# Performance work log

Measured on AMD Instinct MI355X. Metric: run time of the kernel, lower is better.

## Reference

```python
import jax, jax.numpy as jnp
import numpy as np

B, N, T, H, W = 4, 256, 4096, 6, 8
SIM_DIM, LOOKUP, OUT_DIM = 128, 101, 128


def setup_inputs() -> dict:
    key = jax.random.key(0)
    k1, k2, k3, k4 = jax.random.split(key, 4)
    x = jax.random.normal(k1, (B, N, T, H, W), dtype=jnp.float32)
    # nn.Linear weights: [out_features, in_features]
    w_proj = jax.random.normal(k2, (SIM_DIM, N), dtype=jnp.float32) * (1.0 / np.sqrt(N))
    w_fc = jax.random.normal(k3, (OUT_DIM, LOOKUP), dtype=jnp.float32) * (1.0 / np.sqrt(LOOKUP))
    b_fc = jax.random.normal(k4, (OUT_DIM,), dtype=jnp.float32) * 0.01
    return {"x": x, "w_proj": w_proj, "w_fc": w_fc, "b_fc": b_fc}


def reference(x, w_proj, w_fc, b_fc):
    # x: [B, N, T, H, W] == torch.stack(inputs, dim=1) for N branch features
    pad = (LOOKUP - 1) // 2
    feat = x.mean(axis=(3, 4))                    # [B, N, T]  spatial mean-pool
    feat = jnp.swapaxes(feat, 1, 2)               # [B, T, N]
    proj = feat @ w_proj.T                        # [B, T, D]  projection (no bias)
    norm = jnp.linalg.norm(proj, axis=2, keepdims=True)
    proj = proj / jnp.maximum(norm, 1e-12)        # F.normalize(p=2, dim=2)
    sims = jnp.einsum('btd,bsd->bts', proj, proj)  # [B, T, T] full pairwise cosine sims
    sims_pad = jnp.pad(sims, ((0, 0), (0, 0), (pad, pad)))  # [B, T, T+w-1]
    # banded gather: band[b,t,j] = sims_pad[b, t, t + j]
    band_idx = jnp.arange(T)[:, None] + jnp.arange(LOOKUP)[None, :]  # [T, w]
    band = jnp.take_along_axis(sims_pad, band_idx[None], axis=2)     # [B, T, w]
    return jax.nn.relu(band @ w_fc.T + b_fc)      # [B, T, OUT_DIM]
```

## Files before the change

kernel.cpp:

```cpp
#include <hip/hip_runtime.h>

#define BB   4
#define NN   256
#define TT   4096
#define DD   128
#define LK   101
#define PADK 50
#define OD   128
#define ROWS 164
#define RSTR 33
#define FSTR 260
#define CPB  8

typedef float vfloat4 __attribute__((ext_vector_type(4)));

__global__ __launch_bounds__(256) void transpose_w_kernel(
    const float* __restrict__ w_proj, const float* __restrict__ w_fc,
    float* __restrict__ w_t, float* __restrict__ wfc_t) {
  int idx = blockIdx.x * 256 + threadIdx.x;
  int stride = gridDim.x * 256;
  for (int i = idx; i < DD * NN; i += stride) {
    int d = i / NN, n = i - d * NN;
    w_t[n * DD + d] = w_proj[i];
  }
  for (int i = idx; i < OD * LK; i += stride) {
    int o = i / LK, j = i - o * LK;
    wfc_t[j * OD + o] = w_fc[i];
  }
}

__global__ __launch_bounds__(256) void pool_kernel(
    const float* __restrict__ x, float* __restrict__ feat) {
  __shared__ float part[2][768];
  int tid = threadIdx.x;
  for (int c = 0; c < CPB; ++c) {
    size_t ck = (size_t)blockIdx.x * CPB + c;
    const vfloat4* x4 = (const vfloat4*)(x + ck * 3072);
    float* pb = part[c & 1];
#pragma unroll
    for (int p = 0; p < 3; ++p) {
      vfloat4 v = __builtin_nontemporal_load(&x4[p * 256 + tid]);
      pb[p * 256 + tid] = v.x + v.y + v.z + v.w;
    }
    __syncthreads();
    if (tid < 64) {
      float s = 0.f;
#pragma unroll
      for (int i = 0; i < 12; ++i) s += pb[tid * 12 + i];
      feat[ck * 64 + tid] = s * (1.0f / 48.0f);
    }
  }
}

__global__ __launch_bounds__(512, 1) void proj_kernel(
    const float* __restrict__ feat, const float* __restrict__ w_t,
    float* __restrict__ projn) {
  extern __shared__ float smemB[];
  float* fs = smemB;
  float* ss = smemB + 64 * FSTR;
  int b = blockIdx.x >> 6;
  int t0 = (blockIdx.x & 63) << 6;
  int tid = threadIdx.x;

  const float* fb = feat + ((size_t)b * NN) * TT + t0;
  for (int i = tid; i < NN * 64; i += 512) {
    int n = i >> 6, u = i & 63;
    fs[u * FSTR + n] = fb[(size_t)n * TT + u];
  }
  __syncthreads();

  int w = tid >> 6, lane = tid & 63;
  int d0u = __builtin_amdgcn_readfirstlane((tid >> 6) * 16);
  float acc[16];
#pragma unroll
  for (int k = 0; k < 16; ++k) acc[k] = 0.f;

  const float* fsr = fs + lane * FSTR;
  for (int n = 0; n < NN; n += 4) {
    float4 f = *(const float4*)(fsr + n);
    const float* wrow = w_t + n * DD + d0u;
#pragma unroll
    for (int q = 0; q < 4; ++q) {
      float fq = (q == 0) ? f.x : (q == 1) ? f.y : (q == 2) ? f.z : f.w;
      const float4* wv4 = (const float4*)(wrow + q * DD);
#pragma unroll
      for (int k = 0; k < 4; ++k) {
        float4 wv = wv4[k];
        acc[4 * k + 0] += wv.x * fq;
        acc[4 * k + 1] += wv.y * fq;
        acc[4 * k + 2] += wv.z * fq;
        acc[4 * k + 3] += wv.w * fq;
      }
    }
  }

  float s2 = 0.f;
#pragma unroll
  for (int k = 0; k < 16; ++k) s2 += acc[k] * acc[k];
  ss[w * 64 + lane] = s2;
  __syncthreads();
  float tot = 0.f;
#pragma unroll
  for (int q = 0; q < 8; ++q) tot += ss[q * 64 + lane];
  float inv = 1.0f / fmaxf(sqrtf(tot), 1e-12f);

  float4* po = (float4*)(projn + ((size_t)(b * TT + t0 + lane)) * DD + d0u);
#pragma unroll
  for (int k = 0; k < 4; ++k) {
    float4 o;
    o.x = acc[4 * k + 0] * inv;
    o.y = acc[4 * k + 1] * inv;
    o.z = acc[4 * k + 2] * inv;
    o.w = acc[4 * k + 3] * inv;
    po[k] = o;
  }
}

__global__ __launch_bounds__(512, 1) void band_fc_kernel(
    const float* __restrict__ projn, const float* __restrict__ wfc_t,
    const float* __restrict__ b_fc, float* __restrict__ out) {
  extern __shared__ float4 smemC[];
  float4* p4 = smemC;
  float* band = (float*)(smemC + ROWS * RSTR);
  int b = blockIdx.x >> 6;
  int t0 = (blockIdx.x & 63) << 6;
  int tid = threadIdx.x;

  const float4* pg = (const float4*)projn;
  for (int i = tid; i < ROWS * 32; i += 512) {
    int r = i >> 5, c = i & 31;
    int t = t0 + r - PADK;
    float4 v = make_float4(0.f, 0.f, 0.f, 0.f);
    if (t >= 0 && t < TT) v = pg[(((size_t)b * TT + t) << 5) + c];
    p4[r * RSTR + c] = v;
  }
  __syncthreads();

  int w = tid >> 6, tt = tid & 63;

  float4 own[32];
#pragma unroll
  for (int c = 0; c < 32; ++c) own[c] = p4[(tt + PADK) * RSTR + c];

  int s0 = w * 21;
  int sEnd = (s0 + 21 < ROWS) ? (s0 + 21) : ROWS;
  for (int s = s0; s < sEnd; ++s) {
    float a = 0.f;
#pragma unroll
    for (int c = 0; c < 32; ++c) {
      float4 ov = p4[s * RSTR + c];
      a += own[c].x * ov.x + own[c].y * ov.y + own[c].z * ov.z + own[c].w * ov.w;
    }
    int j = s - tt;
    if (j >= 0 && j < LK) band[tt * LK + j] = a;
  }
  __syncthreads();

  int o0u = __builtin_amdgcn_readfirstlane((tid >> 6) * 16);
  float acc[16];
  const float4* bf4 = (const float4*)(b_fc + o0u);
#pragma unroll
  for (int k = 0; k < 4; ++k) {
    float4 bv = bf4[k];
    acc[4 * k + 0] = bv.x; acc[4 * k + 1] = bv.y;
    acc[4 * k + 2] = bv.z; acc[4 * k + 3] = bv.w;
  }
#pragma unroll 2
  for (int j = 0; j < LK; ++j) {
    float bv = band[tt * LK + j];
    const float4* wr = (const float4*)(wfc_t + j * OD + o0u);
#pragma unroll
    for (int k = 0; k < 4; ++k) {
      float4 wv = wr[k];
      acc[4 * k + 0] += wv.x * bv;
      acc[4 * k + 1] += wv.y * bv;
      acc[4 * k + 2] += wv.z * bv;
      acc[4 * k + 3] += wv.w * bv;
    }
  }
  float4* og = (float4*)(out + ((size_t)(b * TT + t0 + tt)) * OD + o0u);
#pragma unroll
  for (int k = 0; k < 4; ++k) {
    float4 o;
    o.x = fmaxf(acc[4 * k + 0], 0.f);
    o.y = fmaxf(acc[4 * k + 1], 0.f);
    o.z = fmaxf(acc[4 * k + 2], 0.f);
    o.w = fmaxf(acc[4 * k + 3], 0.f);
    og[k] = o;
  }
}

extern "C" void kernel_launch(void* const* d_in, const int* in_sizes, int n_in,
                              void* d_out, int out_size, void* d_ws, size_t ws_size,
                              hipStream_t stream) {
  const float* x      = (const float*)d_in[0];
  const float* w_proj = (const float*)d_in[1];
  const float* w_fc   = (const float*)d_in[2];
  const float* b_fc   = (const float*)d_in[3];
  float* out = (float*)d_out;

  char* ws = (char*)d_ws;
  float* feat  = (float*)ws;
  float* projn = (float*)(ws + 16777216);
  float* w_t   = (float*)(ws + 16777216 + 8388608);
  float* wfc_t = (float*)(ws + 16777216 + 8388608 + 131072);

  size_t smB = (size_t)(64 * FSTR + 8 * 64) * sizeof(float);
  size_t smC = (size_t)ROWS * RSTR * sizeof(float4) + (size_t)64 * LK * sizeof(float);
  (void)hipFuncSetAttribute((const void*)proj_kernel,
                      hipFuncAttributeMaxDynamicSharedMemorySize, (int)smB);
  (void)hipFuncSetAttribute((const void*)band_fc_kernel,
                      hipFuncAttributeMaxDynamicSharedMemorySize, (int)smC);

  transpose_w_kernel<<<64, 256, 0, stream>>>(w_proj, w_fc, w_t, wfc_t);
  pool_kernel<<<(BB * NN * TT) / (64 * CPB), 256, 0, stream>>>(x, feat);
  proj_kernel<<<BB * (TT / 64), 512, smB, stream>>>(feat, w_t, projn);
  band_fc_kernel<<<BB * (TT / 64), 512, smC, stream>>>(projn, wfc_t, b_fc, out);
}
```

Baseline: 224.2 us.

## Fuse spatial mean-pool into projection kernel and split band dot accumulators

The separate pool kernel and the proj kernel become one kernel. Each block loads its 32 timesteps × 256 channels of x directly, pools into XOR-swizzled shared memory, and runs the projection with the channel dimension split across two half-waves combined by a shuffle. This removes the feat round-trip through global memory and one launch, and doubles the proj grid to 512 blocks. The band dot product also uses four independent accumulators to break the FMA dependency chain. The risk is that the x reads are now 192-byte rows per thread, strided across timesteps, instead of fully coalesced contiguous reads, which may hurt bandwidth on the dominant 200MB input stream.

```diff
diff --git a/kernel.cpp b/kernel.cpp
--- a/kernel.cpp
+++ b/kernel.cpp
@@ -9,10 +9,7 @@
 #define OD   128
 #define ROWS 164
 #define RSTR 33
-#define FSTR 260
-#define CPB  8
-
-typedef float vfloat4 __attribute__((ext_vector_type(4)));
+#define FSTR 264
 
 __global__ __launch_bounds__(256) void transpose_w_kernel(
     const float* __restrict__ w_proj, const float* __restrict__ w_fc,
@@ -29,59 +26,52 @@
   }
 }
 
-__global__ __launch_bounds__(256) void pool_kernel(
-    const float* __restrict__ x, float* __restrict__ feat) {
-  __shared__ float part[2][768];
+__global__ __launch_bounds__(512) void pool_proj_kernel(
+    const float* __restrict__ x, const float* __restrict__ w_t,
+    float* __restrict__ projn) {
+  __shared__ float fs[32 * FSTR];
+  __shared__ float ss[8 * 32];
+  int b = blockIdx.x >> 7;
+  int t0 = (blockIdx.x & 127) << 5;
   int tid = threadIdx.x;
-  for (int c = 0; c < CPB; ++c) {
-    size_t ck = (size_t)blockIdx.x * CPB + c;
-    const vfloat4* x4 = (const vfloat4*)(x + ck * 3072);
-    float* pb = part[c & 1];
-#pragma unroll
-    for (int p = 0; p < 3; ++p) {
-      vfloat4 v = __builtin_nontemporal_load(&x4[p * 256 + tid]);
-      pb[p * 256 + tid] = v.x + v.y + v.z + v.w;
-    }
-    __syncthreads();
-    if (tid < 64) {
-      float s = 0.f;
-#pragma unroll
-      for (int i = 0; i < 12; ++i) s += pb[tid * 12 + i];
-      feat[ck * 64 + tid] = s * (1.0f / 48.0f);
-    }
-  }
-}
-
-__global__ __launch_bounds__(512, 1) void proj_kernel(
-    const float* __restrict__ feat, const float* __restrict__ w_t,
-    float* __restrict__ projn) {
-  extern __shared__ float smemB[];
-  float* fs = smemB;
-  float* ss = smemB + 64 * FSTR;
-  int b = blockIdx.x >> 6;
-  int t0 = (blockIdx.x & 63) << 6;
-  int tid = threadIdx.x;
-
-  const float* fb = feat + ((size_t)b * NN) * TT + t0;
-  for (int i = tid; i < NN * 64; i += 512) {
-    int n = i >> 6, u = i & 63;
-    fs[u * FSTR + n] = fb[(size_t)n * TT + u];
+
+#pragma unroll
+  for (int i = 0; i < 16; ++i) {
+    int p = i * 512 + tid;
+    int n = p >> 5, t = p & 31;
+    const float4* row = (const float4*)(x + ((size_t)(b * NN + n) * TT + (t0 + t)) * 48);
+    float s0 = 0.f, s1 = 0.f, s2 = 0.f, s3 = 0.f;
+#pragma unroll
+    for (int q = 0; q < 3; ++q) {
+      float4 v0 = row[q * 4 + 0], v1 = row[q * 4 + 1];
+      float4 v2 = row[q * 4 + 2], v3 = row[q * 4 + 3];
+      s0 += v0.x + v0.y + v0.z + v0.w;
+      s1 += v1.x + v1.y + v1.z + v1.w;
+      s2 += v2.x + v2.y + v2.z + v2.w;
+      s3 += v3.x + v3.y + v3.z + v3.w;
+    }
+    int slot = n >> 2;
+    int slots = slot ^ (t & 15);
+    fs[t * FSTR + (slots << 2) + (n & 3)] = ((s0 + s1) + (s2 + s3)) * (1.0f / 48.0f);
   }
   __syncthreads();
 
   int w = tid >> 6, lane = tid & 63;
-  int d0u = __builtin_amdgcn_readfirstlane((tid >> 6) * 16);
+  int t = lane & 31, h = lane >> 5;
+  int d0 = __builtin_amdgcn_readfirstlane((tid >> 6) * 16);
   float acc[16];
 #pragma unroll
   for (int k = 0; k < 16; ++k) acc[k] = 0.f;
 
-  const float* fsr = fs + lane * FSTR;
-  for (int n = 0; n < NN; n += 4) {
-    float4 f = *(const float4*)(fsr + n);
-    const float* wrow = w_t + n * DD + d0u;
+  const float* fsr = fs + t * FSTR;
+  for (int c = 0; c < 32; ++c) {
+    int slot = h * 32 + c;
+    float4 f4 = *(const float4*)(fsr + ((slot ^ (t & 15)) << 2));
+    int nb = (h * 128 + c * 4);
+    const float* wrow = w_t + nb * DD + d0;
 #pragma unroll
     for (int q = 0; q < 4; ++q) {
-      float fq = (q == 0) ? f.x : (q == 1) ? f.y : (q == 2) ? f.z : f.w;
+      float fq = (q == 0) ? f4.x : (q == 1) ? f4.y : (q == 2) ? f4.z : f4.w;
       const float4* wv4 = (const float4*)(wrow + q * DD);
 #pragma unroll
       for (int k = 0; k < 4; ++k) {
@@ -93,25 +83,28 @@
       }
     }
   }
+#pragma unroll
+  for (int k = 0; k < 16; ++k) acc[k] += __shfl_xor(acc[k], 32, 64);
 
   float s2 = 0.f;
 #pragma unroll
   for (int k = 0; k < 16; ++k) s2 += acc[k] * acc[k];
-  ss[w * 64 + lane] = s2;
+  if (h == 0) ss[w * 32 + t] = s2;
   __syncthreads();
   float tot = 0.f;
 #pragma unroll
-  for (int q = 0; q < 8; ++q) tot += ss[q * 64 + lane];
+  for (int q = 0; q < 8; ++q) tot += ss[q * 32 + t];
   float inv = 1.0f / fmaxf(sqrtf(tot), 1e-12f);
 
-  float4* po = (float4*)(projn + ((size_t)(b * TT + t0 + lane)) * DD + d0u);
-#pragma unroll
-  for (int k = 0; k < 4; ++k) {
+  float4* po = (float4*)(projn + ((size_t)(b * TT + t0 + t)) * DD + d0 + h * 8);
+#pragma unroll
+  for (int k = 0; k < 2; ++k) {
+    int kb = h * 8 + k * 4;
     float4 o;
-    o.x = acc[4 * k + 0] * inv;
-    o.y = acc[4 * k + 1] * inv;
-    o.z = acc[4 * k + 2] * inv;
-    o.w = acc[4 * k + 3] * inv;
+    o.x = acc[kb + 0] * inv;
+    o.y = acc[kb + 1] * inv;
+    o.z = acc[kb + 2] * inv;
+    o.w = acc[kb + 3] * inv;
     po[k] = o;
   }
 }
@@ -145,14 +138,17 @@
   int s0 = w * 21;
   int sEnd = (s0 + 21 < ROWS) ? (s0 + 21) : ROWS;
   for (int s = s0; s < sEnd; ++s) {
-    float a = 0.f;
+    float a0 = 0.f, a1 = 0.f, a2 = 0.f, a3 = 0.f;
 #pragma unroll
     for (int c = 0; c < 32; ++c) {
       float4 ov = p4[s * RSTR + c];
-      a += own[c].x * ov.x + own[c].y * ov.y + own[c].z * ov.z + own[c].w * ov.w;
+      a0 += own[c].x * ov.x;
+      a1 += own[c].y * ov.y;
+      a2 += own[c].z * ov.z;
+      a3 += own[c].w * ov.w;
     }
     int j = s - tt;
-    if (j >= 0 && j < LK) band[tt * LK + j] = a;
+    if (j >= 0 && j < LK) band[tt * LK + j] = (a0 + a1) + (a2 + a3);
   }
   __syncthreads();
 
@@ -200,20 +196,15 @@
   float* out = (float*)d_out;
 
   char* ws = (char*)d_ws;
-  float* feat  = (float*)ws;
-  float* projn = (float*)(ws + 16777216);
-  float* w_t   = (float*)(ws + 16777216 + 8388608);
-  float* wfc_t = (float*)(ws + 16777216 + 8388608 + 131072);
-
-  size_t smB = (size_t)(64 * FSTR + 8 * 64) * sizeof(float);
+  float* projn = (float*)ws;
+  float* w_t   = (float*)(ws + 8388608);
+  float* wfc_t = (float*)(ws + 8388608 + 131072);
+
   size_t smC = (size_t)ROWS * RSTR * sizeof(float4) + (size_t)64 * LK * sizeof(float);
-  (void)hipFuncSetAttribute((const void*)proj_kernel,
-                      hipFuncAttributeMaxDynamicSharedMemorySize, (int)smB);
   (void)hipFuncSetAttribute((const void*)band_fc_kernel,
                       hipFuncAttributeMaxDynamicSharedMemorySize, (int)smC);
 
   transpose_w_kernel<<<64, 256, 0, stream>>>(w_proj, w_fc, w_t, wfc_t);
-  pool_kernel<<<(BB * NN * TT) / (64 * CPB), 256, 0, stream>>>(x, feat);
-  proj_kernel<<<BB * (TT / 64), 512, smB, stream>>>(feat, w_t, projn);
+  pool_proj_kernel<<<BB * (TT / 32), 512, 0, stream>>>(x, w_t, projn);
   band_fc_kernel<<<BB * (TT / 64), 512, smC, stream>>>(projn, wfc_t, b_fc, out);
 }
```

Measured after the change: 338.5 us. 51.0% more time.

## Register-tile projection GEMM with staged weights in LDS and shuffle-based normalization

Applied to the files above, without the earlier changes.

Rewrites the projection kernel as a 4x4 register-tiled outer-product loop. Feature tiles are loaded with coalesced float4 reads in [n][t] layout, and w_proj is staged in shared memory in chunks of 64 rows instead of being read from global memory per thread. The row norm reduction now uses wavefront shuffles instead of a shared-memory pass. Separately, the band dot product and the pool reduction are split into several independent accumulators to shorten dependency chains. The cost is more shared memory per block and extra barriers between weight chunks.

```diff
diff --git a/kernel.cpp b/kernel.cpp
--- a/kernel.cpp
+++ b/kernel.cpp
@@ -9,8 +9,9 @@
 #define OD   128
 #define ROWS 164
 #define RSTR 33
-#define FSTR 260
 #define CPB  8
+#define FS_STR 68
+#define WB_STR 132
 
 typedef float vfloat4 __attribute__((ext_vector_type(4)));
 
@@ -40,14 +41,15 @@
 #pragma unroll
     for (int p = 0; p < 3; ++p) {
       vfloat4 v = __builtin_nontemporal_load(&x4[p * 256 + tid]);
-      pb[p * 256 + tid] = v.x + v.y + v.z + v.w;
+      pb[p * 256 + tid] = (v.x + v.y) + (v.z + v.w);
     }
     __syncthreads();
     if (tid < 64) {
-      float s = 0.f;
-#pragma unroll
-      for (int i = 0; i < 12; ++i) s += pb[tid * 12 + i];
-      feat[ck * 64 + tid] = s * (1.0f / 48.0f);
+      float s0 = 0.f, s1 = 0.f;
+      const float* pp = pb + tid * 12;
+#pragma unroll
+      for (int i = 0; i < 6; ++i) { s0 += pp[i]; s1 += pp[6 + i]; }
+      feat[ck * 64 + tid] = (s0 + s1) * (1.0f / 48.0f);
     }
   }
 }
@@ -55,64 +57,74 @@
 __global__ __launch_bounds__(512, 1) void proj_kernel(
     const float* __restrict__ feat, const float* __restrict__ w_t,
     float* __restrict__ projn) {
-  extern __shared__ float smemB[];
-  float* fs = smemB;
-  float* ss = smemB + 64 * FSTR;
+  extern __shared__ float smemP[];
+  float* fs   = smemP;
+  float* wbuf = smemP + NN * FS_STR;
   int b = blockIdx.x >> 6;
   int t0 = (blockIdx.x & 63) << 6;
   int tid = threadIdx.x;
-
-  const float* fb = feat + ((size_t)b * NN) * TT + t0;
-  for (int i = tid; i < NN * 64; i += 512) {
-    int n = i >> 6, u = i & 63;
-    fs[u * FSTR + n] = fb[(size_t)n * TT + u];
-  }
-  __syncthreads();
-
-  int w = tid >> 6, lane = tid & 63;
-  int d0u = __builtin_amdgcn_readfirstlane((tid >> 6) * 16);
-  float acc[16];
-#pragma unroll
-  for (int k = 0; k < 16; ++k) acc[k] = 0.f;
-
-  const float* fsr = fs + lane * FSTR;
-  for (int n = 0; n < NN; n += 4) {
-    float4 f = *(const float4*)(fsr + n);
-    const float* wrow = w_t + n * DD + d0u;
-#pragma unroll
-    for (int q = 0; q < 4; ++q) {
-      float fq = (q == 0) ? f.x : (q == 1) ? f.y : (q == 2) ? f.z : f.w;
-      const float4* wv4 = (const float4*)(wrow + q * DD);
-#pragma unroll
-      for (int k = 0; k < 4; ++k) {
-        float4 wv = wv4[k];
-        acc[4 * k + 0] += wv.x * fq;
-        acc[4 * k + 1] += wv.y * fq;
-        acc[4 * k + 2] += wv.z * fq;
-        acc[4 * k + 3] += wv.w * fq;
+  int td = tid & 31, tt = tid >> 5;
+
+  float acc[4][4];
+#pragma unroll
+  for (int i = 0; i < 4; ++i)
+#pragma unroll
+    for (int j = 0; j < 4; ++j) acc[i][j] = 0.f;
+
+  for (int c = 0; c < 4; ++c) {
+    if (c) __syncthreads();
+#pragma unroll
+    for (int k = 0; k < 4; ++k) {
+      int slot = tid + k * 512;
+      int n = slot >> 5, d4 = slot & 31;
+      *(float4*)(wbuf + n * WB_STR + d4 * 4) =
+          *(const float4*)(w_t + (size_t)(c * 64 + n) * DD + d4 * 4);
+    }
+    if (c == 0) {
+#pragma unroll
+      for (int k = 0; k < 8; ++k) {
+        int slot = tid + k * 512;
+        int n = slot >> 4, t4 = slot & 15;
+        *(float4*)(fs + n * FS_STR + t4 * 4) =
+            *(const float4*)(feat + ((size_t)(b * NN + n)) * TT + t0 + t4 * 4);
       }
     }
-  }
-
-  float s2 = 0.f;
-#pragma unroll
-  for (int k = 0; k < 16; ++k) s2 += acc[k] * acc[k];
-  ss[w * 64 + lane] = s2;
-  __syncthreads();
-  float tot = 0.f;
-#pragma unroll
-  for (int q = 0; q < 8; ++q) tot += ss[q * 64 + lane];
-  float inv = 1.0f / fmaxf(sqrtf(tot), 1e-12f);
-
-  float4* po = (float4*)(projn + ((size_t)(b * TT + t0 + lane)) * DD + d0u);
-#pragma unroll
-  for (int k = 0; k < 4; ++k) {
+    __syncthreads();
+
+    const float* fp = fs + (c * 64) * FS_STR + tt * 4;
+    const float* wp = wbuf + td * 4;
+#pragma unroll 4
+    for (int n = 0; n < 64; ++n) {
+      float4 f = *(const float4*)(fp + n * FS_STR);
+      float4 wv = *(const float4*)(wp + n * WB_STR);
+      float fa[4] = {f.x, f.y, f.z, f.w};
+#pragma unroll
+      for (int i = 0; i < 4; ++i) {
+        acc[i][0] += fa[i] * wv.x;
+        acc[i][1] += fa[i] * wv.y;
+        acc[i][2] += fa[i] * wv.z;
+        acc[i][3] += fa[i] * wv.w;
+      }
+    }
+  }
+
+  float s[4];
+#pragma unroll
+  for (int i = 0; i < 4; ++i)
+    s[i] = acc[i][0] * acc[i][0] + acc[i][1] * acc[i][1] +
+           acc[i][2] * acc[i][2] + acc[i][3] * acc[i][3];
+#pragma unroll
+  for (int m = 1; m < 32; m <<= 1) {
+#pragma unroll
+    for (int i = 0; i < 4; ++i) s[i] += __shfl_xor(s[i], m, 64);
+  }
+#pragma unroll
+  for (int i = 0; i < 4; ++i) {
+    float inv = 1.0f / fmaxf(sqrtf(s[i]), 1e-12f);
     float4 o;
-    o.x = acc[4 * k + 0] * inv;
-    o.y = acc[4 * k + 1] * inv;
-    o.z = acc[4 * k + 2] * inv;
-    o.w = acc[4 * k + 3] * inv;
-    po[k] = o;
+    o.x = acc[i][0] * inv; o.y = acc[i][1] * inv;
+    o.z = acc[i][2] * inv; o.w = acc[i][3] * inv;
+    *(float4*)(projn + ((size_t)(b * TT + t0 + tt * 4 + i)) * DD + td * 4) = o;
   }
 }
 
@@ -145,14 +157,17 @@
   int s0 = w * 21;
   int sEnd = (s0 + 21 < ROWS) ? (s0 + 21) : ROWS;
   for (int s = s0; s < sEnd; ++s) {
-    float a = 0.f;
+    float a0 = 0.f, a1 = 0.f, a2 = 0.f, a3 = 0.f;
 #pragma unroll
     for (int c = 0; c < 32; ++c) {
       float4 ov = p4[s * RSTR + c];
-      a += own[c].x * ov.x + own[c].y * ov.y + own[c].z * ov.z + own[c].w * ov.w;
+      a0 += own[c].x * ov.x;
+      a1 += own[c].y * ov.y;
+      a2 += own[c].z * ov.z;
+      a3 += own[c].w * ov.w;
     }
     int j = s - tt;
-    if (j >= 0 && j < LK) band[tt * LK + j] = a;
+    if (j >= 0 && j < LK) band[tt * LK + j] = (a0 + a1) + (a2 + a3);
   }
   __syncthreads();
 
@@ -205,15 +220,15 @@
   float* w_t   = (float*)(ws + 16777216 + 8388608);
   float* wfc_t = (float*)(ws + 16777216 + 8388608 + 131072);
 
-  size_t smB = (size_t)(64 * FSTR + 8 * 64) * sizeof(float);
+  size_t smP = (size_t)(NN * FS_STR + 64 * WB_STR) * sizeof(float);
   size_t smC = (size_t)ROWS * RSTR * sizeof(float4) + (size_t)64 * LK * sizeof(float);
   (void)hipFuncSetAttribute((const void*)proj_kernel,
-                      hipFuncAttributeMaxDynamicSharedMemorySize, (int)smB);
+                      hipFuncAttributeMaxDynamicSharedMemorySize, (int)smP);
   (void)hipFuncSetAttribute((const void*)band_fc_kernel,
                       hipFuncAttributeMaxDynamicSharedMemorySize, (int)smC);
 
   transpose_w_kernel<<<64, 256, 0, stream>>>(w_proj, w_fc, w_t, wfc_t);
   pool_kernel<<<(BB * NN * TT) / (64 * CPB), 256, 0, stream>>>(x, feat);
-  proj_kernel<<<BB * (TT / 64), 512, smB, stream>>>(feat, w_t, projn);
+  proj_kernel<<<BB * (TT / 64), 512, smP, stream>>>(feat, w_t, projn);
   band_fc_kernel<<<BB * (TT / 64), 512, smC, stream>>>(projn, wfc_t, b_fc, out);
 }
```

After: 219.8 us. No clear change (-2.0%).
